# Performance work log

Hardware: AMD Instinct MI355X
Metric: run time of the kernel (lower is better)

The kernel has to match this reference:

```python
import jax, jax.numpy as jnp
import numpy as np

NUM_ITERATIONS = 4


def setup_inputs() -> dict:
    key = jax.random.key(0)
    k1, k2, k3, k4 = jax.random.split(key, 4)
    N, F, G = 100000, 512, 1000
    x = jax.random.normal(k1, (N, F), dtype=jnp.float32)
    node_graph_index = jnp.sort(jax.random.randint(k2, (N,), 0, G, dtype=jnp.int64))
    # Keras LSTM params: kernel [input_dim=2F, 4F], recurrent_kernel [F, 4F], bias [4F]
    kernel = jax.random.normal(k3, (2 * F, 4 * F), dtype=jnp.float32) * 0.05
    recurrent_kernel = jax.random.normal(k4, (F, 4 * F), dtype=jnp.float32) * 0.05
    bias = jnp.zeros((4 * F,), dtype=jnp.float32)
    return {"x": x, "node_graph_index": node_graph_index, "kernel": kernel,
            "recurrent_kernel": recurrent_kernel, "bias": bias, "num_graphs": G}


def _lstm_step(q_star, h, c, kernel, recurrent_kernel, bias, F):
    # Keras gate order: i, f, g (cell candidate), o
    z = q_star @ kernel + h @ recurrent_kernel + bias  # [G, 4F]
    i = jax.nn.sigmoid(z[:, 0 * F:1 * F])
    f = jax.nn.sigmoid(z[:, 1 * F:2 * F])
    g = jnp.tanh(z[:, 2 * F:3 * F])
    o = jax.nn.sigmoid(z[:, 3 * F:4 * F])
    c_new = f * c + i * g
    h_new = o * jnp.tanh(c_new)
    return h_new, c_new


def reference(x, node_graph_index, kernel, recurrent_kernel, bias, num_graphs):
    F = x.shape[-1]
    G = num_graphs
    idx = node_graph_index
    h = jnp.zeros((G, F), dtype=x.dtype)
    c = jnp.zeros((G, F), dtype=x.dtype)
    q_star = jnp.zeros((G, 2 * F), dtype=x.dtype)
    for _ in range(NUM_ITERATIONS):
        h, c = _lstm_step(q_star, h, c, kernel, recurrent_kernel, bias, F)
        q = h  # [G, F]
        # attention logits per node: <x_n, q_{graph(n)}>
        e = jnp.einsum('nf,nf->n', x, q[idx])  # [N]
        # segment softmax over nodes of each graph (numerically stable)
        emax = jax.ops.segment_max(e, idx, num_segments=G)
        emax = jnp.where(jnp.isfinite(emax), emax, 0.0)  # empty segments
        ee = jnp.exp(e - emax[idx])
        denom = jax.ops.segment_sum(ee, idx, num_segments=G)
        a = ee / jnp.where(denom == 0, 1.0, denom)[idx]  # [N]
        # weighted scatter-sum readout
        r = jax.ops.segment_sum(a[:, None] * x, idx, num_segments=G)  # [G, F]
        q_star = jnp.concatenate([q, r], axis=-1)  # [G, 2F]
    return q_star
```

## Files before the change

kernel.cpp:

```cpp
#include <hip/hip_runtime.h>
#include <cmath>
#include <cstdint>

#define FF   512
#define G4F  2048
#define G2F  1024
#define KTOT 1536
#define MPAD 1024
#define NITER 4

typedef __attribute__((ext_vector_type(8))) short bf16x8;
typedef __attribute__((ext_vector_type(4))) float f32x4;

__device__ __forceinline__ ushort f2bf(float x) {
  uint32_t u = __float_as_uint(x);
  return (ushort)((u + 0x7FFFu + ((u >> 16) & 1u)) >> 16);
}
__device__ __forceinline__ float bf2f(ushort b) {
  return __uint_as_float(((uint32_t)b) << 16);
}

__global__ void seg_bounds_kernel(const int* __restrict__ idx, int N,
                                  int* __restrict__ segs, int* __restrict__ sege) {
  int n = blockIdx.x * blockDim.x + threadIdx.x;
  if (n >= N) return;
  int g = idx[n];
  if (n == 0     || idx[n-1] != g) segs[g] = n;
  if (n == N-1   || idx[n+1] != g) sege[g] = n + 1;
}

__global__ __launch_bounds__(256) void prep_w_kernel(
    const float* __restrict__ Wk, const float* __restrict__ Wr,
    ushort* __restrict__ Wt_hi, ushort* __restrict__ Wt_lo) {
  __shared__ float t[32][33];
  int k0 = blockIdx.x * 32;
  int n0 = blockIdx.y * 32;
  int tx = threadIdx.x & 31, ty = threadIdx.x >> 5;
  #pragma unroll
  for (int i = 0; i < 4; ++i) {
    int k = k0 + ty + 8 * i;
    const float* srow = (k < 1024) ? (Wk + (size_t)k * 2048)
                                   : (Wr + (size_t)(k - 1024) * 2048);
    t[ty + 8 * i][tx] = srow[n0 + tx];
  }
  __syncthreads();
  #pragma unroll
  for (int i = 0; i < 4; ++i) {
    int r = ty + 8 * i;
    float v = t[tx][r];
    ushort hi = f2bf(v);
    ushort lo = f2bf(v - bf2f(hi));
    size_t o = (size_t)(n0 + r) * KTOT + k0 + tx;
    Wt_hi[o] = hi;
    Wt_lo[o] = lo;
  }
}

__global__ __launch_bounds__(256) void prep_a_kernel(
    const float* __restrict__ qstar, const float* __restrict__ h,
    ushort* __restrict__ A_hi, ushort* __restrict__ A_lo, int G) {
  int i = blockIdx.x * blockDim.x + threadIdx.x;
  int perRow = KTOT / 4;
  if (i >= G * perRow) return;
  int row = i / perRow;
  int c4  = (i - row * perRow) * 4;
  const float* src = (c4 < G2F) ? (qstar + (size_t)row * G2F + c4)
                                : (h     + (size_t)row * FF  + (c4 - G2F));
  float4 v = *(const float4*)src;
  ushort4 hh, ll;
  hh.x = f2bf(v.x); ll.x = f2bf(v.x - bf2f(hh.x));
  hh.y = f2bf(v.y); ll.y = f2bf(v.y - bf2f(hh.y));
  hh.z = f2bf(v.z); ll.z = f2bf(v.z - bf2f(hh.z));
  hh.w = f2bf(v.w); ll.w = f2bf(v.w - bf2f(hh.w));
  size_t o = (size_t)row * KTOT + c4;
  *(ushort4*)(A_hi + o) = hh;
  *(ushort4*)(A_lo + o) = ll;
}

#define GBM 64
#define GBN 64
#define GBK 32
#define LDP 40

__global__ __launch_bounds__(256) void gemm_mfma_kernel(
    const ushort* __restrict__ A_hi, const ushort* __restrict__ A_lo,
    const ushort* __restrict__ Wt_hi, const ushort* __restrict__ Wt_lo,
    float* __restrict__ z) {
  __shared__ ushort Ah[GBM][LDP], Al[GBM][LDP], Bh[GBN][LDP], Bl[GBN][LDP];

  int row0 = blockIdx.x * GBM;
  int col0 = blockIdx.y * GBN;
  int tid  = threadIdx.x, lane = tid & 63, wid = tid >> 6;
  int wr = wid >> 1, wc = wid & 1;
  int sr = tid >> 2, sk = (tid & 3) * 8;

  const ushort* pa_h = A_hi  + (size_t)(row0 + sr) * KTOT + sk;
  const ushort* pa_l = A_lo  + (size_t)(row0 + sr) * KTOT + sk;
  const ushort* pb_h = Wt_hi + (size_t)(col0 + sr) * KTOT + sk;
  const ushort* pb_l = Wt_lo + (size_t)(col0 + sr) * KTOT + sk;

  f32x4 acc[2][2] = {};

  for (int k0 = 0; k0 < KTOT; k0 += GBK) {
    bf16x8 va_h = *(const bf16x8*)(pa_h + k0);
    bf16x8 va_l = *(const bf16x8*)(pa_l + k0);
    bf16x8 vb_h = *(const bf16x8*)(pb_h + k0);
    bf16x8 vb_l = *(const bf16x8*)(pb_l + k0);
    *(bf16x8*)&Ah[sr][sk] = va_h;
    *(bf16x8*)&Al[sr][sk] = va_l;
    *(bf16x8*)&Bh[sr][sk] = vb_h;
    *(bf16x8*)&Bl[sr][sk] = vb_l;
    __syncthreads();

    int ar = wr * 32 + (lane & 15);
    int bc = wc * 32 + (lane & 15);
    int ko = (lane >> 4) * 8;
    bf16x8 ah[2], al[2], bh[2], bl[2];
    ah[0] = *(const bf16x8*)&Ah[ar][ko];      al[0] = *(const bf16x8*)&Al[ar][ko];
    ah[1] = *(const bf16x8*)&Ah[ar + 16][ko]; al[1] = *(const bf16x8*)&Al[ar + 16][ko];
    bh[0] = *(const bf16x8*)&Bh[bc][ko];      bl[0] = *(const bf16x8*)&Bl[bc][ko];
    bh[1] = *(const bf16x8*)&Bh[bc + 16][ko]; bl[1] = *(const bf16x8*)&Bl[bc + 16][ko];

    #pragma unroll
    for (int mr = 0; mr < 2; ++mr)
      #pragma unroll
      for (int nc = 0; nc < 2; ++nc) {
        acc[mr][nc] = __builtin_amdgcn_mfma_f32_16x16x32_bf16(ah[mr], bh[nc], acc[mr][nc], 0, 0, 0);
        acc[mr][nc] = __builtin_amdgcn_mfma_f32_16x16x32_bf16(ah[mr], bl[nc], acc[mr][nc], 0, 0, 0);
        acc[mr][nc] = __builtin_amdgcn_mfma_f32_16x16x32_bf16(al[mr], bh[nc], acc[mr][nc], 0, 0, 0);
      }
    __syncthreads();
  }

  int cr = (lane >> 4) * 4, cc = lane & 15;
  #pragma unroll
  for (int mr = 0; mr < 2; ++mr)
    #pragma unroll
    for (int nc = 0; nc < 2; ++nc) {
      float* zp = z + (size_t)(row0 + wr * 32 + mr * 16 + cr) * G4F
                    + col0 + wc * 32 + nc * 16 + cc;
      #pragma unroll
      for (int r = 0; r < 4; ++r) zp[(size_t)r * G4F] = acc[mr][nc][r];
    }
}

__global__ __launch_bounds__(256) void gates_kernel(
    const float* __restrict__ z, const float* __restrict__ bias,
    float* __restrict__ h, float* __restrict__ c, float* __restrict__ qs,
    int G, int zero_z) {
  int i = blockIdx.x * blockDim.x + threadIdx.x;
  if (i >= G * FF) return;
  int g = i >> 9;
  int j = i & (FF - 1);
  float zi = bias[j], zf = bias[FF + j], zg = bias[2*FF + j], zo = bias[3*FF + j];
  float cold = 0.f;
  if (!zero_z) {
    const float* zr = z + (size_t)g * G4F;
    zi += zr[j]; zf += zr[FF + j]; zg += zr[2*FF + j]; zo += zr[3*FF + j];
    cold = c[i];
  }
  float ig = 1.f / (1.f + expf(-zi));
  float fg = 1.f / (1.f + expf(-zf));
  float gg = tanhf(zg);
  float og = 1.f / (1.f + expf(-zo));
  float cn = fg * cold + ig * gg;
  float hn = og * tanhf(cn);
  c[i] = cn;
  h[i] = hn;
  qs[(size_t)g * G2F + j] = hn;
}

__device__ __forceinline__ float dotq_reduce(const float4& a0, const float4& a1,
                                             const float4& q0, const float4& q1) {
  float p = a0.x*q0.x + a0.y*q0.y + a0.z*q0.z + a0.w*q0.w
          + a1.x*q1.x + a1.y*q1.y + a1.z*q1.z + a1.w*q1.w;
  #pragma unroll
  for (int off = 32; off; off >>= 1) p += __shfl_xor(p, off);
  return p;
}

__global__ __launch_bounds__(256) void attn_fused_kernel(
    const float* __restrict__ x, const float* __restrict__ h,
    const int* __restrict__ segs, const int* __restrict__ sege,
    float* __restrict__ qs_out) {
  int g = blockIdx.x;
  int s = segs[g], e = sege[g];
  int tid = threadIdx.x, wid = tid >> 6, lane = tid & 63;

  __shared__ float wm[4], wd[4];
  __shared__ float wr[4][FF];

  float4 q0, q1;
  {
    const float* hp = h + (size_t)g * FF;
    q0 = *(const float4*)(hp + 4 * lane);
    q1 = *(const float4*)(hp + 256 + 4 * lane);
  }

  float m = -INFINITY, d = 0.f;
  float4 r0 = make_float4(0.f, 0.f, 0.f, 0.f);
  float4 r1 = make_float4(0.f, 0.f, 0.f, 0.f);

  auto upd = [&](float p, const float4& a0, const float4& a1) {
    if (p > m) {
      float sc = __expf(m - p);
      d *= sc;
      r0.x *= sc; r0.y *= sc; r0.z *= sc; r0.w *= sc;
      r1.x *= sc; r1.y *= sc; r1.z *= sc; r1.w *= sc;
      m = p;
    }
    float w = __expf(p - m);
    d += w;
    r0.x += w * a0.x; r0.y += w * a0.y; r0.z += w * a0.z; r0.w += w * a0.w;
    r1.x += w * a1.x; r1.y += w * a1.y; r1.z += w * a1.z; r1.w += w * a1.w;
  };

  int i = s + wid;
  for (; i + 4 < e; i += 8) {
    const float* xa = x + (size_t)i * FF;
    const float* xb = x + (size_t)(i + 4) * FF;
    float4 a0 = *(const float4*)(xa + 4 * lane);
    float4 a1 = *(const float4*)(xa + 256 + 4 * lane);
    float4 b0 = *(const float4*)(xb + 4 * lane);
    float4 b1 = *(const float4*)(xb + 256 + 4 * lane);
    float pa = dotq_reduce(a0, a1, q0, q1);
    float pb = dotq_reduce(b0, b1, q0, q1);
    upd(pa, a0, a1);
    upd(pb, b0, b1);
  }
  if (i < e) {
    const float* xa = x + (size_t)i * FF;
    float4 a0 = *(const float4*)(xa + 4 * lane);
    float4 a1 = *(const float4*)(xa + 256 + 4 * lane);
    float pa = dotq_reduce(a0, a1, q0, q1);
    upd(pa, a0, a1);
  }

  if (lane == 0) { wm[wid] = m; wd[wid] = d; }
  *(float4*)&wr[wid][4 * lane]       = r0;
  *(float4*)&wr[wid][256 + 4 * lane] = r1;
  __syncthreads();

  float m0 = wm[0], m1 = wm[1], m2 = wm[2], m3 = wm[3];
  float ms = fmaxf(fmaxf(m0, m1), fmaxf(m2, m3));
  float s0 = (m0 == -INFINITY) ? 0.f : __expf(m0 - ms);
  float s1 = (m1 == -INFINITY) ? 0.f : __expf(m1 - ms);
  float s2 = (m2 == -INFINITY) ? 0.f : __expf(m2 - ms);
  float s3 = (m3 == -INFINITY) ? 0.f : __expf(m3 - ms);
  float dt = wd[0]*s0 + wd[1]*s1 + wd[2]*s2 + wd[3]*s3;
  float inv = (dt > 0.f) ? 1.f / dt : 0.f;

  int cc = tid * 2;
  float2 v0 = *(float2*)&wr[0][cc];
  float2 v1 = *(float2*)&wr[1][cc];
  float2 v2 = *(float2*)&wr[2][cc];
  float2 v3 = *(float2*)&wr[3][cc];
  float rx = (v0.x*s0 + v1.x*s1 + v2.x*s2 + v3.x*s3) * inv;
  float ry = (v0.y*s0 + v1.y*s1 + v2.y*s2 + v3.y*s3) * inv;
  *(float2*)(qs_out + (size_t)g * G2F + FF + cc) = make_float2(rx, ry);
}

extern "C" void kernel_launch(void* const* d_in, const int* in_sizes, int n_in,
                              void* d_out, int out_size, void* d_ws, size_t ws_size,
                              hipStream_t stream) {
  const float* x    = (const float*)d_in[0];
  const int*   idx  = (const int*)d_in[1];
  const float* Wk   = (const float*)d_in[2];
  const float* Wr   = (const float*)d_in[3];
  const float* bias = (const float*)d_in[4];
  int N = in_sizes[1];
  int F = in_sizes[4] / 4;
  int G = out_size / (2 * F);
  (void)n_in; (void)ws_size; (void)F;

  float* qstar = (float*)d_out;

  char* p = (char*)d_ws;
  float*  h     = (float*)p;            p += (size_t)G * FF * 4;
  float*  c     = (float*)p;            p += (size_t)G * FF * 4;
  float*  z     = (float*)p;            p += (size_t)MPAD * G4F * 4;
  ushort* A_hi  = (ushort*)p;           p += (size_t)MPAD * KTOT * 2;
  ushort* A_lo  = (ushort*)p;           p += (size_t)MPAD * KTOT * 2;
  ushort* Wt_hi = (ushort*)p;           p += (size_t)G4F * KTOT * 2;
  ushort* Wt_lo = (ushort*)p;           p += (size_t)G4F * KTOT * 2;
  int*    segs  = (int*)p;              p += (size_t)G * 4;
  int*    sege  = (int*)p;

  hipMemsetAsync(segs, 0, 2 * sizeof(int) * (size_t)G, stream);
  seg_bounds_kernel<<<(N + 255) / 256, 256, 0, stream>>>(idx, N, segs, sege);

  prep_w_kernel<<<dim3(KTOT / 32, G4F / 32), 256, 0, stream>>>(Wk, Wr, Wt_hi, Wt_lo);

  dim3 ggrid((G + GBM - 1) / GBM, G4F / GBN);

  for (int it = 0; it < NITER; ++it) {
    if (it == 0) {
      gates_kernel<<<(G * FF + 255) / 256, 256, 0, stream>>>(z, bias, h, c, qstar, G, 1);
    } else {
      prep_a_kernel<<<(G * (KTOT / 4) + 255) / 256, 256, 0, stream>>>(qstar, h, A_hi, A_lo, G);
      gemm_mfma_kernel<<<ggrid, 256, 0, stream>>>(A_hi, A_lo, Wt_hi, Wt_lo, z);
      gates_kernel<<<(G * FF + 255) / 256, 256, 0, stream>>>(z, bias, h, c, qstar, G, 0);
    }
    attn_fused_kernel<<<G, 256, 0, stream>>>(x, h, segs, sege, qstar);
  }
}
```

Before: 548.3 us.

## Fold recurrent weights into kernel, fuse A-prep into gates/attn, block attention rows

Because q_star's first half equals h after every step, the recurrent kernel is added into the first 512 rows of the input kernel, which shrinks the GEMM K dimension from 1536 to 1024. The separate prep_a kernel is removed: the gates and attention kernels now write the bf16 hi/lo split of h and r directly into the GEMM A buffers. The attention kernel gives each wave a contiguous chunk of nodes and does the online softmax four rows at a time with one rescale per batch, replacing the per-row branchy update. Summing the weights before the bf16 split changes rounding slightly.

```diff
diff --git a/kernel.cpp b/kernel.cpp
--- a/kernel.cpp
+++ b/kernel.cpp
@@ -5,7 +5,7 @@
 #define FF   512
 #define G4F  2048
 #define G2F  1024
-#define KTOT 1536
+#define KC   1024
 #define MPAD 1024
 #define NITER 4
 
@@ -39,9 +39,9 @@
   #pragma unroll
   for (int i = 0; i < 4; ++i) {
     int k = k0 + ty + 8 * i;
-    const float* srow = (k < 1024) ? (Wk + (size_t)k * 2048)
-                                   : (Wr + (size_t)(k - 1024) * 2048);
-    t[ty + 8 * i][tx] = srow[n0 + tx];
+    float v = Wk[(size_t)k * 2048 + n0 + tx];
+    if (k < 512) v += Wr[(size_t)k * 2048 + n0 + tx];
+    t[ty + 8 * i][tx] = v;
   }
   __syncthreads();
   #pragma unroll
@@ -50,31 +50,10 @@
     float v = t[tx][r];
     ushort hi = f2bf(v);
     ushort lo = f2bf(v - bf2f(hi));
-    size_t o = (size_t)(n0 + r) * KTOT + k0 + tx;
+    size_t o = (size_t)(n0 + r) * KC + k0 + tx;
     Wt_hi[o] = hi;
     Wt_lo[o] = lo;
   }
-}
-
-__global__ __launch_bounds__(256) void prep_a_kernel(
-    const float* __restrict__ qstar, const float* __restrict__ h,
-    ushort* __restrict__ A_hi, ushort* __restrict__ A_lo, int G) {
-  int i = blockIdx.x * blockDim.x + threadIdx.x;
-  int perRow = KTOT / 4;
-  if (i >= G * perRow) return;
-  int row = i / perRow;
-  int c4  = (i - row * perRow) * 4;
-  const float* src = (c4 < G2F) ? (qstar + (size_t)row * G2F + c4)
-                                : (h     + (size_t)row * FF  + (c4 - G2F));
-  float4 v = *(const float4*)src;
-  ushort4 hh, ll;
-  hh.x = f2bf(v.x); ll.x = f2bf(v.x - bf2f(hh.x));
-  hh.y = f2bf(v.y); ll.y = f2bf(v.y - bf2f(hh.y));
-  hh.z = f2bf(v.z); ll.z = f2bf(v.z - bf2f(hh.z));
-  hh.w = f2bf(v.w); ll.w = f2bf(v.w - bf2f(hh.w));
-  size_t o = (size_t)row * KTOT + c4;
-  *(ushort4*)(A_hi + o) = hh;
-  *(ushort4*)(A_lo + o) = ll;
 }
 
 #define GBM 64
@@ -94,14 +73,14 @@
   int wr = wid >> 1, wc = wid & 1;
   int sr = tid >> 2, sk = (tid & 3) * 8;
 
-  const ushort* pa_h = A_hi  + (size_t)(row0 + sr) * KTOT + sk;
-  const ushort* pa_l = A_lo  + (size_t)(row0 + sr) * KTOT + sk;
-  const ushort* pb_h = Wt_hi + (size_t)(col0 + sr) * KTOT + sk;
-  const ushort* pb_l = Wt_lo + (size_t)(col0 + sr) * KTOT + sk;
+  const ushort* pa_h = A_hi  + (size_t)(row0 + sr) * KC + sk;
+  const ushort* pa_l = A_lo  + (size_t)(row0 + sr) * KC + sk;
+  const ushort* pb_h = Wt_hi + (size_t)(col0 + sr) * KC + sk;
+  const ushort* pb_l = Wt_lo + (size_t)(col0 + sr) * KC + sk;
 
   f32x4 acc[2][2] = {};
 
-  for (int k0 = 0; k0 < KTOT; k0 += GBK) {
+  for (int k0 = 0; k0 < KC; k0 += GBK) {
     bf16x8 va_h = *(const bf16x8*)(pa_h + k0);
     bf16x8 va_l = *(const bf16x8*)(pa_l + k0);
     bf16x8 vb_h = *(const bf16x8*)(pb_h + k0);
@@ -147,6 +126,7 @@
 __global__ __launch_bounds__(256) void gates_kernel(
     const float* __restrict__ z, const float* __restrict__ bias,
     float* __restrict__ h, float* __restrict__ c, float* __restrict__ qs,
+    ushort* __restrict__ A_hi, ushort* __restrict__ A_lo,
     int G, int zero_z) {
   int i = blockIdx.x * blockDim.x + threadIdx.x;
   if (i >= G * FF) return;
@@ -168,6 +148,9 @@
   c[i] = cn;
   h[i] = hn;
   qs[(size_t)g * G2F + j] = hn;
+  ushort hh = f2bf(hn), ll = f2bf(hn - bf2f(hh));
+  A_hi[(size_t)g * KC + j] = hh;
+  A_lo[(size_t)g * KC + j] = ll;
 }
 
 __device__ __forceinline__ float dotq_reduce(const float4& a0, const float4& a1,
@@ -182,13 +165,14 @@
 __global__ __launch_bounds__(256) void attn_fused_kernel(
     const float* __restrict__ x, const float* __restrict__ h,
     const int* __restrict__ segs, const int* __restrict__ sege,
-    float* __restrict__ qs_out) {
+    float* __restrict__ qs_out,
+    ushort* __restrict__ A_hi, ushort* __restrict__ A_lo) {
   int g = blockIdx.x;
   int s = segs[g], e = sege[g];
   int tid = threadIdx.x, wid = tid >> 6, lane = tid & 63;
 
   __shared__ float wm[4], wd[4];
-  __shared__ float wr[4][FF];
+  __shared__ float wrs[4][FF];
 
   float4 q0, q1;
   {
@@ -197,48 +181,66 @@
     q1 = *(const float4*)(hp + 256 + 4 * lane);
   }
 
+  int len = e - s;
+  int qlen = (len + 3) >> 2;
+  int i0 = s + wid * qlen;
+  int i1 = i0 + qlen; if (i1 > e) i1 = e;
+
   float m = -INFINITY, d = 0.f;
   float4 r0 = make_float4(0.f, 0.f, 0.f, 0.f);
   float4 r1 = make_float4(0.f, 0.f, 0.f, 0.f);
 
-  auto upd = [&](float p, const float4& a0, const float4& a1) {
-    if (p > m) {
-      float sc = __expf(m - p);
-      d *= sc;
-      r0.x *= sc; r0.y *= sc; r0.z *= sc; r0.w *= sc;
-      r1.x *= sc; r1.y *= sc; r1.z *= sc; r1.w *= sc;
-      m = p;
-    }
-    float w = __expf(p - m);
-    d += w;
-    r0.x += w * a0.x; r0.y += w * a0.y; r0.z += w * a0.z; r0.w += w * a0.w;
-    r1.x += w * a1.x; r1.y += w * a1.y; r1.z += w * a1.z; r1.w += w * a1.w;
-  };
-
-  int i = s + wid;
-  for (; i + 4 < e; i += 8) {
-    const float* xa = x + (size_t)i * FF;
-    const float* xb = x + (size_t)(i + 4) * FF;
-    float4 a0 = *(const float4*)(xa + 4 * lane);
-    float4 a1 = *(const float4*)(xa + 256 + 4 * lane);
-    float4 b0 = *(const float4*)(xb + 4 * lane);
-    float4 b1 = *(const float4*)(xb + 256 + 4 * lane);
-    float pa = dotq_reduce(a0, a1, q0, q1);
-    float pb = dotq_reduce(b0, b1, q0, q1);
-    upd(pa, a0, a1);
-    upd(pb, b0, b1);
-  }
-  if (i < e) {
-    const float* xa = x + (size_t)i * FF;
-    float4 a0 = *(const float4*)(xa + 4 * lane);
-    float4 a1 = *(const float4*)(xa + 256 + 4 * lane);
-    float pa = dotq_reduce(a0, a1, q0, q1);
-    upd(pa, a0, a1);
+  int i = i0;
+  for (; i + 4 <= i1; i += 4) {
+    const float* xp = x + (size_t)i * FF + 4 * lane;
+    float4 a00 = *(const float4*)(xp);
+    float4 a01 = *(const float4*)(xp + 256);
+    float4 a10 = *(const float4*)(xp + FF);
+    float4 a11 = *(const float4*)(xp + FF + 256);
+    float4 a20 = *(const float4*)(xp + 2*FF);
+    float4 a21 = *(const float4*)(xp + 2*FF + 256);
+    float4 a30 = *(const float4*)(xp + 3*FF);
+    float4 a31 = *(const float4*)(xp + 3*FF + 256);
+    float p0 = dotq_reduce(a00, a01, q0, q1);
+    float p1 = dotq_reduce(a10, a11, q0, q1);
+    float p2 = dotq_reduce(a20, a21, q0, q1);
+    float p3 = dotq_reduce(a30, a31, q0, q1);
+    float mnew = fmaxf(fmaxf(m, fmaxf(p0, p1)), fmaxf(p2, p3));
+    float sc = __expf(m - mnew);
+    float w0 = __expf(p0 - mnew);
+    float w1 = __expf(p1 - mnew);
+    float w2 = __expf(p2 - mnew);
+    float w3 = __expf(p3 - mnew);
+    d = d * sc + ((w0 + w1) + (w2 + w3));
+    r0.x = r0.x*sc + w0*a00.x + w1*a10.x + w2*a20.x + w3*a30.x;
+    r0.y = r0.y*sc + w0*a00.y + w1*a10.y + w2*a20.y + w3*a30.y;
+    r0.z = r0.z*sc + w0*a00.z + w1*a10.z + w2*a20.z + w3*a30.z;
+    r0.w = r0.w*sc + w0*a00.w + w1*a10.w + w2*a20.w + w3*a30.w;
+    r1.x = r1.x*sc + w0*a01.x + w1*a11.x + w2*a21.x + w3*a31.x;
+    r1.y = r1.y*sc + w0*a01.y + w1*a11.y + w2*a21.y + w3*a31.y;
+    r1.z = r1.z*sc + w0*a01.z + w1*a11.z + w2*a21.z + w3*a31.z;
+    r1.w = r1.w*sc + w0*a01.w + w1*a11.w + w2*a21.w + w3*a31.w;
+    m = mnew;
+  }
+  for (; i < i1; ++i) {
+    const float* xp = x + (size_t)i * FF + 4 * lane;
+    float4 a0 = *(const float4*)(xp);
+    float4 a1 = *(const float4*)(xp + 256);
+    float p = dotq_reduce(a0, a1, q0, q1);
+    float mnew = fmaxf(m, p);
+    float sc = __expf(m - mnew);
+    float w  = __expf(p - mnew);
+    d = d * sc + w;
+    r0.x = r0.x*sc + w*a0.x; r0.y = r0.y*sc + w*a0.y;
+    r0.z = r0.z*sc + w*a0.z; r0.w = r0.w*sc + w*a0.w;
+    r1.x = r1.x*sc + w*a1.x; r1.y = r1.y*sc + w*a1.y;
+    r1.z = r1.z*sc + w*a1.z; r1.w = r1.w*sc + w*a1.w;
+    m = mnew;
   }
 
   if (lane == 0) { wm[wid] = m; wd[wid] = d; }
-  *(float4*)&wr[wid][4 * lane]       = r0;
-  *(float4*)&wr[wid][256 + 4 * lane] = r1;
+  *(float4*)&wrs[wid][4 * lane]       = r0;
+  *(float4*)&wrs[wid][256 + 4 * lane] = r1;
   __syncthreads();
 
   float m0 = wm[0], m1 = wm[1], m2 = wm[2], m3 = wm[3];
@@ -251,13 +253,19 @@
   float inv = (dt > 0.f) ? 1.f / dt : 0.f;
 
   int cc = tid * 2;
-  float2 v0 = *(float2*)&wr[0][cc];
-  float2 v1 = *(float2*)&wr[1][cc];
-  float2 v2 = *(float2*)&wr[2][cc];
-  float2 v3 = *(float2*)&wr[3][cc];
+  float2 v0 = *(float2*)&wrs[0][cc];
+  float2 v1 = *(float2*)&wrs[1][cc];
+  float2 v2 = *(float2*)&wrs[2][cc];
+  float2 v3 = *(float2*)&wrs[3][cc];
   float rx = (v0.x*s0 + v1.x*s1 + v2.x*s2 + v3.x*s3) * inv;
   float ry = (v0.y*s0 + v1.y*s1 + v2.y*s2 + v3.y*s3) * inv;
   *(float2*)(qs_out + (size_t)g * G2F + FF + cc) = make_float2(rx, ry);
+
+  ushort2 hh, ll;
+  hh.x = f2bf(rx); ll.x = f2bf(rx - bf2f(hh.x));
+  hh.y = f2bf(ry); ll.y = f2bf(ry - bf2f(hh.y));
+  *(ushort2*)(A_hi + (size_t)g * KC + FF + cc) = hh;
+  *(ushort2*)(A_lo + (size_t)g * KC + FF + cc) = ll;
 }
 
 extern "C" void kernel_launch(void* const* d_in, const int* in_sizes, int n_in,
@@ -279,28 +287,27 @@
   float*  h     = (float*)p;            p += (size_t)G * FF * 4;
   float*  c     = (float*)p;            p += (size_t)G * FF * 4;
   float*  z     = (float*)p;            p += (size_t)MPAD * G4F * 4;
-  ushort* A_hi  = (ushort*)p;           p += (size_t)MPAD * KTOT * 2;
-  ushort* A_lo  = (ushort*)p;           p += (size_t)MPAD * KTOT * 2;
-  ushort* Wt_hi = (ushort*)p;           p += (size_t)G4F * KTOT * 2;
-  ushort* Wt_lo = (ushort*)p;           p += (size_t)G4F * KTOT * 2;
+  ushort* A_hi  = (ushort*)p;           p += (size_t)MPAD * KC * 2;
+  ushort* A_lo  = (ushort*)p;           p += (size_t)MPAD * KC * 2;
+  ushort* Wt_hi = (ushort*)p;           p += (size_t)G4F * KC * 2;
+  ushort* Wt_lo = (ushort*)p;           p += (size_t)G4F * KC * 2;
   int*    segs  = (int*)p;              p += (size_t)G * 4;
   int*    sege  = (int*)p;
 
   hipMemsetAsync(segs, 0, 2 * sizeof(int) * (size_t)G, stream);
   seg_bounds_kernel<<<(N + 255) / 256, 256, 0, stream>>>(idx, N, segs, sege);
 
-  prep_w_kernel<<<dim3(KTOT / 32, G4F / 32), 256, 0, stream>>>(Wk, Wr, Wt_hi, Wt_lo);
+  prep_w_kernel<<<dim3(KC / 32, G4F / 32), 256, 0, stream>>>(Wk, Wr, Wt_hi, Wt_lo);
 
   dim3 ggrid((G + GBM - 1) / GBM, G4F / GBN);
 
   for (int it = 0; it < NITER; ++it) {
     if (it == 0) {
-      gates_kernel<<<(G * FF + 255) / 256, 256, 0, stream>>>(z, bias, h, c, qstar, G, 1);
+      gates_kernel<<<(G * FF + 255) / 256, 256, 0, stream>>>(z, bias, h, c, qstar, A_hi, A_lo, G, 1);
     } else {
-      prep_a_kernel<<<(G * (KTOT / 4) + 255) / 256, 256, 0, stream>>>(qstar, h, A_hi, A_lo, G);
       gemm_mfma_kernel<<<ggrid, 256, 0, stream>>>(A_hi, A_lo, Wt_hi, Wt_lo, z);
-      gates_kernel<<<(G * FF + 255) / 256, 256, 0, stream>>>(z, bias, h, c, qstar, G, 0);
+      gates_kernel<<<(G * FF + 255) / 256, 256, 0, stream>>>(z, bias, h, c, qstar, A_hi, A_lo, G, 0);
     }
-    attn_fused_kernel<<<G, 256, 0, stream>>>(x, h, segs, sege, qstar);
-  }
-}
+    attn_fused_kernel<<<G, 256, 0, stream>>>(x, h, segs, sege, qstar, A_hi, A_lo);
+  }
+}
```

New measurement: 503.0 us. 1.09x faster.
